# Performance work log

Measured on AMD Instinct MI355X. Metric: run time of the kernel, lower is better.

## Reference

```python
import jax, jax.numpy as jnp
import numpy as np

DIM = 512
MOVE_EMBED_DIM = 64
NUM_BUCKETS = 64
EMBED = 768
B = 8192
STEPS = 10


def setup_inputs() -> dict:
    key = jax.random.key(0)
    ks = jax.random.split(key, 16)
    def g(i, shape, scale=0.02):
        return jax.random.normal(ks[i], shape, jnp.float32) * scale
    return {
        "boards": jax.random.normal(ks[0], (STEPS, B, EMBED), jnp.float32),
        "flags": jax.random.randint(ks[1], (STEPS - 2, B), 0, 2).astype(bool),
        "themes": jax.random.randint(ks[2], (B,), 0, 10),
        "moves": jax.random.randint(ks[3], (B,), 0, NUM_BUCKETS),
        "start": jax.random.uniform(ks[4], (DIM,), jnp.float32),
        "red_w": g(5, (DIM, EMBED)), "red_b": jnp.zeros((DIM,), jnp.float32),
        "ca_w": g(6, (DIM, DIM)), "ca_b": jnp.zeros((DIM,), jnp.float32),
        "cb_w": g(7, (DIM, DIM)), "cb_b": jnp.zeros((DIM,), jnp.float32),
        "move_emb": g(8, (NUM_BUCKETS, MOVE_EMBED_DIM), 1.0),
        "fc1_w": g(9, (DIM, DIM + MOVE_EMBED_DIM)), "fc1_b": jnp.zeros((DIM,), jnp.float32),
        "fc2_w": g(10, (DIM, DIM)), "fc2_b": jnp.zeros((DIM,), jnp.float32),
        "fc3_w": g(11, (1024, DIM)), "fc3_b": jnp.zeros((1024,), jnp.float32),
        "fc4_w": g(12, (1024, 1024)), "fc4_b": jnp.zeros((1024,), jnp.float32),
        "fc5_w": g(13, (512, 1024)), "fc5_b": jnp.zeros((512,), jnp.float32),
        "out_w": g(14, (1, 512)), "out_b": jnp.zeros((1,), jnp.float32),
    }


def reference(boards, flags, themes, moves, start, red_w, red_b, ca_w, ca_b,
              cb_w, cb_b, move_emb, fc1_w, fc1_b, fc2_w, fc2_b, fc3_w, fc3_b,
              fc4_w, fc4_b, fc5_w, fc5_b, out_w, out_b):
    bsz = boards.shape[1]
    # boards[0:2] are never masked; boards[2:10] are zeroed where flags are False
    full_flags = jnp.concatenate([jnp.ones((2, bsz), bool), flags], axis=0)  # [10,B]
    emb = jnp.where(full_flags[:, :, None], boards, 0.0)                     # [10,B,E]
    # shared dim reducer + relu applied to all 10 positions at once
    e = jax.nn.relu(jnp.einsum('sbe,de->sbd', emb, red_w) + red_b)           # [10,B,DIM]
    # precompute combiner_b contribution for every step (batched GEMM)
    eb = jnp.einsum('sbd,kd->sbk', e, cb_w) + cb_b                           # [10,B,DIM]
    # combiner_a(start)+combiner_b(e0) == combiner_a(h0)+... with h0 = start broadcast
    h0 = jnp.broadcast_to(start, (bsz, DIM))
    def step(h, eb_t):
        return jnp.tanh(h @ ca_w.T + ca_b + eb_t), None
    h, _ = jax.lax.scan(step, h0, eb)                                        # [B,DIM]
    # dropout layers are identity in eval mode
    m = move_emb[moves]                                                      # [B,MOVE_EMBED_DIM]
    x = jax.nn.relu(jnp.concatenate([h, m], axis=-1) @ fc1_w.T + fc1_b)
    x = jax.nn.relu(x @ fc2_w.T + fc2_b)
    x = jax.nn.relu(x @ fc3_w.T + fc3_b)
    x = jax.nn.relu(x @ fc4_w.T + fc4_b)
    x = jax.nn.relu(x @ fc5_w.T + fc5_b)
    return x @ out_w.T + out_b                                               # [B,1]
```

## Files before the change

kernel.cpp:

```cpp
#include <hip/hip_runtime.h>
#include <math.h>

#define BATCH  8192
#define EMBED  768
#define DIMD   512
#define MEDIM  64
#define NSTEP  10

typedef __bf16 bf16x8 __attribute__((ext_vector_type(8)));
typedef float  f32x4  __attribute__((ext_vector_type(4)));

__device__ __forceinline__ void load16_lds(const void* g, void* l)
{
    auto* gp = (__attribute__((address_space(1))) char*)(uintptr_t)g;
    auto* lp = (__attribute__((address_space(3))) char*)(unsigned int)(uintptr_t)l;
    __builtin_amdgcn_global_load_lds(gp, lp, 16, 0, 0);
}

#define WAITV(n) asm volatile("s_waitcnt vmcnt(" #n ")" ::: "memory")

#define BN 128
#define BK 32

template<int ACT, bool ADDEB, bool GATHER, int BMT>
__global__ __launch_bounds__(256)
void gemm_bf16(const __bf16* __restrict__ A, const __bf16* __restrict__ Bt,
               const float* __restrict__ bias, const __bf16* __restrict__ add,
               const __bf16* __restrict__ me, const int* __restrict__ moves,
               __bf16* __restrict__ C, int M, int N, int K)
{
    constexpr int NG = (BMT + BN) / 16;
    constexpr int AG = BMT / 16;
    constexpr int MR = BMT / 32;
    constexpr int NC = NG / 4;

    __shared__ __bf16 lds[3][(BMT + BN) * BK];

    const int nwg  = gridDim.x * gridDim.y;
    const int orig = blockIdx.y * gridDim.x + blockIdx.x;
    const int cpx  = nwg >> 3;
    const int swz  = (orig & 7) * cpx + (orig >> 3);
    const int bx   = swz % gridDim.x;
    const int by   = swz / gridDim.x;

    const int tid  = threadIdx.x;
    const int wave = tid >> 6;
    const int lane = tid & 63;
    const int row0 = by * BMT;
    const int col0 = bx * BN;

    const int wr = (wave >> 1) * (BMT / 2);
    const int wc = (wave & 1) * 64;
    const int fr = lane & 15;
    const int q  = lane >> 4;

    const int srow = lane >> 2;
    const int skk  = (((lane & 3) ^ ((lane >> 3) & 3)) * 8);

    int mv[2] = {0, 0};
    if (GATHER) {
#pragma unroll
        for (int ci = 0; ci < 2; ++ci)
            mv[ci] = moves[row0 + (ci * 4 + wave) * 16 + srow];
    }

    auto stage_one = [&](int buf, int k0, int ci) {
        const int c = ci * 4 + wave;
        const int r = c * 16 + srow;
        const __bf16* g;
        if (c < AG) {
            if (GATHER) {
                g = (k0 < DIMD)
                    ? (A  + (size_t)(row0 + r) * DIMD + k0 + skk)
                    : (me + (size_t)mv[ci] * MEDIM + (k0 - DIMD) + skk);
            } else {
                g = A + (size_t)(row0 + r) * K + k0 + skk;
            }
        } else {
            g = Bt + (size_t)(col0 + (r - BMT)) * K + k0 + skk;
        }
        load16_lds(g, &lds[buf][c * 512]);
    };
    auto stage = [&](int buf, int k0) {
#pragma unroll
        for (int ci = 0; ci < NC; ++ci) stage_one(buf, k0, ci);
    };

    auto frag = [&](const __bf16* base, int r) -> bf16x8 {
        return *(const bf16x8*)&base[r * 32 + ((q ^ ((r >> 1) & 3)) << 3)];
    };

    f32x4 acc[MR][4] = {};

    const int NT = K / BK;
    stage(0, 0);
    stage(1, BK);

    int rd = 0;
    for (int t = 0; t < NT; ++t) {
        if (t + 1 < NT) {
            if constexpr (NC == 4) WAITV(4); else WAITV(3);
        } else {
            WAITV(0);
        }
        __builtin_amdgcn_s_barrier();
        __builtin_amdgcn_sched_barrier(0);

        const bool dost = (t + 2 < NT);
        int wrb = rd + 2; if (wrb >= 3) wrb -= 3;
        const int k0s = (t + 2) * BK;

        const __bf16* As = lds[rd];
        const __bf16* Bs = lds[rd] + BMT * BK;
        bf16x8 bfr[4];
#pragma unroll
        for (int n = 0; n < 4; ++n)
            bfr[n] = frag(Bs, wc + n * 16 + fr);

        __builtin_amdgcn_s_setprio(1);
#pragma unroll
        for (int m = 0; m < MR; ++m) {
            if (dost) {
#pragma unroll
                for (int ci = m * NC / MR; ci < (m + 1) * NC / MR; ++ci)
                    stage_one(wrb, k0s, ci);
            }
            const bf16x8 af = frag(As, wr + m * 16 + fr);
#pragma unroll
            for (int n = 0; n < 4; ++n)
                acc[m][n] = __builtin_amdgcn_mfma_f32_16x16x32_bf16(
                                af, bfr[n], acc[m][n], 0, 0, 0);
        }
        __builtin_amdgcn_s_setprio(0);

        __builtin_amdgcn_s_barrier();
        __builtin_amdgcn_sched_barrier(0);
        ++rd; if (rd >= 3) rd -= 3;
    }

#pragma unroll
    for (int m = 0; m < MR; ++m) {
#pragma unroll
        for (int n = 0; n < 4; ++n) {
            const int cc = col0 + wc + n * 16 + fr;
            const float bb = bias[cc];
#pragma unroll
            for (int j = 0; j < 4; ++j) {
                const int rr = row0 + wr + m * 16 + (lane >> 4) * 4 + j;
                float v = acc[m][n][j] + bb;
                if (ADDEB) v += (float)add[(size_t)rr * N + cc];
                if (ACT == 1) v = fmaxf(v, 0.0f);
                if (ACT == 2) {
                    const float p = __expf(2.0f * v);
                    v = 1.0f - 2.0f / (p + 1.0f);
                }
                C[(size_t)rr * N + cc] = (__bf16)v;
            }
        }
    }
}

template<int ACT, bool H1>
__global__ __launch_bounds__(512)
void gemm256(const __bf16* __restrict__ A, const __bf16* __restrict__ Bt,
             const float* __restrict__ bias, const float* __restrict__ tmp,
             __bf16* __restrict__ h1out, __bf16* __restrict__ C,
             int M, int N, int K)
{
    __shared__ __bf16 lds[3][(256 + 128) * 32];

    const int nwg  = gridDim.x * gridDim.y;
    const int orig = blockIdx.y * gridDim.x + blockIdx.x;
    const int cpx  = nwg >> 3;
    const int swz  = (orig & 7) * cpx + (orig >> 3);
    const int bx   = swz % gridDim.x;
    const int by   = swz / gridDim.x;

    const int tid  = threadIdx.x;
    const int wave = tid >> 6;
    const int lane = tid & 63;
    const int row0 = by * 256;
    const int col0 = bx * 128;

    const int wr = (wave >> 1) * 64;
    const int wc = (wave & 1) * 64;
    const int fr = lane & 15;
    const int q  = lane >> 4;

    const int srow = lane >> 2;
    const int skk  = (((lane & 3) ^ ((lane >> 3) & 3)) * 8);

    auto stage_one = [&](int buf, int k0, int ci) {
        const int c = ci * 8 + wave;
        const int r = c * 16 + srow;
        const __bf16* g = (c < 16)
            ? (A  + (size_t)(row0 + r) * K + k0 + skk)
            : (Bt + (size_t)(col0 + (r - 256)) * K + k0 + skk);
        load16_lds(g, &lds[buf][c * 512]);
    };
    auto stage = [&](int buf, int k0) {
#pragma unroll
        for (int ci = 0; ci < 3; ++ci) stage_one(buf, k0, ci);
    };

    auto frag = [&](const __bf16* base, int r) -> bf16x8 {
        return *(const bf16x8*)&base[r * 32 + ((q ^ ((r >> 1) & 3)) << 3)];
    };

    f32x4 acc[4][4] = {};

    const int NT = K / BK;
    stage(0, 0);
    stage(1, BK);

    int rd = 0;
    for (int t = 0; t < NT; ++t) {
        if (t + 1 < NT) WAITV(3); else WAITV(0);
        __builtin_amdgcn_s_barrier();
        __builtin_amdgcn_sched_barrier(0);

        const bool dost = (t + 2 < NT);
        int wrb = rd + 2; if (wrb >= 3) wrb -= 3;
        const int k0s = (t + 2) * BK;

        const __bf16* As = lds[rd];
        const __bf16* Bs = lds[rd] + 256 * 32;
        bf16x8 bfr[4];
#pragma unroll
        for (int n = 0; n < 4; ++n)
            bfr[n] = frag(Bs, wc + n * 16 + fr);

        __builtin_amdgcn_s_setprio(1);
#pragma unroll
        for (int m = 0; m < 4; ++m) {
            if (dost) {
#pragma unroll
                for (int ci = m * 3 / 4; ci < (m + 1) * 3 / 4; ++ci)
                    stage_one(wrb, k0s, ci);
            }
            const bf16x8 af = frag(As, wr + m * 16 + fr);
#pragma unroll
            for (int n = 0; n < 4; ++n)
                acc[m][n] = __builtin_amdgcn_mfma_f32_16x16x32_bf16(
                                af, bfr[n], acc[m][n], 0, 0, 0);
        }
        __builtin_amdgcn_s_setprio(0);

        __builtin_amdgcn_s_barrier();
        __builtin_amdgcn_sched_barrier(0);
        ++rd; if (rd >= 3) rd -= 3;
    }

#pragma unroll
    for (int m = 0; m < 4; ++m) {
#pragma unroll
        for (int n = 0; n < 4; ++n) {
            const int cc = col0 + wc + n * 16 + fr;
            const float bb = bias[cc];
#pragma unroll
            for (int j = 0; j < 4; ++j) {
                const int rr = row0 + wr + m * 16 + (lane >> 4) * 4 + j;
                float v = acc[m][n][j] + bb;
                if (ACT == 1) v = fmaxf(v, 0.0f);
                if (H1 && rr < BATCH) {
                    const float vv = v + tmp[cc];
                    const float p = __expf(2.0f * vv);
                    h1out[(size_t)rr * N + cc] = (__bf16)(1.0f - 2.0f / (p + 1.0f));
                } else {
                    C[(size_t)rr * N + cc] = (__bf16)v;
                }
            }
        }
    }
}

enum : int { W_RED = 0, W_CA = 393216, W_CB = 655360, W_FC1 = 917504,
             W_FC2 = 1212416, W_FC3 = 1474560, W_FC4 = 1998848,
             W_FC5 = 3047424, W_ME = 3571712, W_TOTAL = 3575808 };

#define NB_BOARDS 30720
#define NB_W      1746
__global__ __launch_bounds__(256)
void prep(const float* __restrict__ boards, const int* __restrict__ flags,
          __bf16* __restrict__ b_all,
          const float* __restrict__ w0, const float* __restrict__ w1,
          const float* __restrict__ w2, const float* __restrict__ w3,
          const float* __restrict__ w4, const float* __restrict__ w5,
          const float* __restrict__ w6, const float* __restrict__ w7,
          const float* __restrict__ w8, __bf16* __restrict__ wpool,
          const float* __restrict__ cab, const float* __restrict__ start,
          float* __restrict__ tmp)
{
    const int bid = blockIdx.x;
    if (bid < NB_BOARDS) {
        const int idx  = bid * 256 + threadIdx.x;
        const int grow = idx / 96;
        const int s    = grow >> 13;
        const int b    = grow & 8191;
        float m = 1.0f;
        if (s >= 2) m = flags[(size_t)(s - 2) * BATCH + b] ? 1.0f : 0.0f;
        const float4 v0 = ((const float4*)boards)[(size_t)idx * 2];
        const float4 v1 = ((const float4*)boards)[(size_t)idx * 2 + 1];
        bf16x8 o;
        o[0] = (__bf16)(v0.x * m); o[1] = (__bf16)(v0.y * m);
        o[2] = (__bf16)(v0.z * m); o[3] = (__bf16)(v0.w * m);
        o[4] = (__bf16)(v1.x * m); o[5] = (__bf16)(v1.y * m);
        o[6] = (__bf16)(v1.z * m); o[7] = (__bf16)(v1.w * m);
        *(bf16x8*)(b_all + (size_t)idx * 8) = o;
    } else if (bid < NB_BOARDS + NB_W) {
        const int idx = (bid - NB_BOARDS) * 256 + threadIdx.x;
        if (idx >= W_TOTAL / 8) return;
        const int e = idx * 8;
        const float* src; int off;
        if      (e < W_CA)  { src = w0; off = W_RED; }
        else if (e < W_CB)  { src = w1; off = W_CA; }
        else if (e < W_FC1) { src = w2; off = W_CB; }
        else if (e < W_FC2) { src = w3; off = W_FC1; }
        else if (e < W_FC3) { src = w4; off = W_FC2; }
        else if (e < W_FC4) { src = w5; off = W_FC3; }
        else if (e < W_FC5) { src = w6; off = W_FC4; }
        else if (e < W_ME)  { src = w7; off = W_FC5; }
        else                { src = w8; off = W_ME; }
        const float4 v0 = ((const float4*)(src + (e - off)))[0];
        const float4 v1 = ((const float4*)(src + (e - off)))[1];
        bf16x8 o;
        o[0] = (__bf16)v0.x; o[1] = (__bf16)v0.y; o[2] = (__bf16)v0.z; o[3] = (__bf16)v0.w;
        o[4] = (__bf16)v1.x; o[5] = (__bf16)v1.y; o[6] = (__bf16)v1.z; o[7] = (__bf16)v1.w;
        *(bf16x8*)(wpool + (size_t)e) = o;
    } else {
        __shared__ float s[DIMD];
        for (int i = threadIdx.x; i < DIMD; i += 256) s[i] = start[i];
        __syncthreads();
        const int n = (bid - NB_BOARDS - NB_W) * 256 + threadIdx.x;
        const float4* w = (const float4*)(w1 + (size_t)n * DIMD);
        float acc = 0.0f;
#pragma unroll 8
        for (int k = 0; k < DIMD / 4; ++k) {
            const float4 wv = w[k];
            acc += wv.x * s[k * 4] + wv.y * s[k * 4 + 1] +
                   wv.z * s[k * 4 + 2] + wv.w * s[k * 4 + 3];
        }
        tmp[n] = acc + cab[n];
    }
}

__global__ __launch_bounds__(256)
void out_head(const __bf16* __restrict__ x, const float* __restrict__ out_w,
              const float* __restrict__ out_b, float* __restrict__ out)
{
    const int wid  = threadIdx.x >> 6;
    const int lane = threadIdx.x & 63;
    const int row  = blockIdx.x * 4 + wid;
    const bf16x8 xv = *(const bf16x8*)(x + (size_t)row * DIMD + lane * 8);
    const float4 w0 = ((const float4*)out_w)[lane * 2];
    const float4 w1 = ((const float4*)out_w)[lane * 2 + 1];
    float s = (float)xv[0] * w0.x + (float)xv[1] * w0.y + (float)xv[2] * w0.z +
              (float)xv[3] * w0.w + (float)xv[4] * w1.x + (float)xv[5] * w1.y +
              (float)xv[6] * w1.z + (float)xv[7] * w1.w;
#pragma unroll
    for (int off = 32; off; off >>= 1) s += __shfl_down(s, off, 64);
    if (lane == 0) out[row] = s + out_b[0];
}

extern "C" void kernel_launch(void* const* d_in, const int* in_sizes, int n_in,
                              void* d_out, int out_size, void* d_ws, size_t ws_size,
                              hipStream_t stream)
{
    const float* boards  = (const float*)d_in[0];
    const int*   flags   = (const int*)  d_in[1];
    const int*   moves   = (const int*)  d_in[3];
    const float* start   = (const float*)d_in[4];
    const float* red_w   = (const float*)d_in[5];
    const float* red_b   = (const float*)d_in[6];
    const float* ca_w    = (const float*)d_in[7];
    const float* ca_b    = (const float*)d_in[8];
    const float* cb_w    = (const float*)d_in[9];
    const float* cb_b    = (const float*)d_in[10];
    const float* move_emb= (const float*)d_in[11];
    const float* fc1_w   = (const float*)d_in[12];
    const float* fc1_b   = (const float*)d_in[13];
    const float* fc2_w   = (const float*)d_in[14];
    const float* fc2_b   = (const float*)d_in[15];
    const float* fc3_w   = (const float*)d_in[16];
    const float* fc3_b   = (const float*)d_in[17];
    const float* fc4_w   = (const float*)d_in[18];
    const float* fc4_b   = (const float*)d_in[19];
    const float* fc5_w   = (const float*)d_in[20];
    const float* fc5_b   = (const float*)d_in[21];
    const float* out_w   = (const float*)d_in[22];
    const float* out_b   = (const float*)d_in[23];

    __bf16* wsb = (__bf16*)d_ws;
    __bf16* wpool  = wsb;
    __bf16* b_all  = wsb + 3575808;
    __bf16* e_all  = wsb + 66490368;
    __bf16* eb_all = wsb + 108433408;
    __bf16* hA     = wsb + 150376448;
    __bf16* hB     = wsb + 154570752;
    float*  tmpv   = (float*)(wsb + 158765056);
    __bf16* x1     = wsb + 159789056;
    __bf16* x2     = wsb + 163983360;
    __bf16* x3     = wsb + 168177664;
    __bf16* x4     = wsb + 176566272;
    __bf16* x5     = wsb + 184954880;

    const dim3 blk(256);

    prep<<<NB_BOARDS + NB_W + 2, blk, 0, stream>>>(
        boards, flags, b_all,
        red_w, ca_w, cb_w, fc1_w, fc2_w, fc3_w, fc4_w, fc5_w, move_emb, wpool,
        ca_b, start, tmpv);

    gemm256<1, false><<<dim3(4, 320), dim3(512), 0, stream>>>(
        b_all, wpool + W_RED, red_b, nullptr, nullptr, e_all,
        NSTEP * BATCH, DIMD, EMBED);
    gemm256<0, true><<<dim3(4, 320), dim3(512), 0, stream>>>(
        e_all, wpool + W_CB, cb_b, tmpv, hA, eb_all,
        NSTEP * BATCH, DIMD, DIMD);

    __bf16* hcur = hA;
    __bf16* hnxt = hB;
    for (int s = 1; s < NSTEP; ++s) {
        const __bf16* ebs = eb_all + (size_t)s * BATCH * DIMD;
        gemm_bf16<2, true, false, 64><<<dim3(4, 128), blk, 0, stream>>>(
            hcur, wpool + W_CA, ca_b, ebs, nullptr, nullptr, hnxt,
            BATCH, DIMD, DIMD);
        __bf16* t = hcur; hcur = hnxt; hnxt = t;
    }

    gemm_bf16<1, false, true, 128><<<dim3(4, 64), blk, 0, stream>>>(
        hcur, wpool + W_FC1, fc1_b, nullptr, wpool + W_ME, moves, x1,
        BATCH, DIMD, DIMD + MEDIM);
    gemm_bf16<1, false, false, 128><<<dim3(4, 64), blk, 0, stream>>>(
        x1, wpool + W_FC2, fc2_b, nullptr, nullptr, nullptr, x2, BATCH, DIMD, DIMD);
    gemm_bf16<1, false, false, 128><<<dim3(8, 64), blk, 0, stream>>>(
        x2, wpool + W_FC3, fc3_b, nullptr, nullptr, nullptr, x3, BATCH, 1024, DIMD);
    gemm_bf16<1, false, false, 128><<<dim3(8, 64), blk, 0, stream>>>(
        x3, wpool + W_FC4, fc4_b, nullptr, nullptr, nullptr, x4, BATCH, 1024, 1024);
    gemm_bf16<1, false, false, 128><<<dim3(4, 64), blk, 0, stream>>>(
        x4, wpool + W_FC5, fc5_b, nullptr, nullptr, nullptr, x5, BATCH, DIMD, 1024);

    out_head<<<BATCH / 4, blk, 0, stream>>>(x5, out_w, out_b, (float*)d_out);
}
```

Measured before the change: 437.7 us.

## Use 256x256-tile ping-pong GEMM kernel for the board reducer

Adds a new gemm8p kernel with 256x256 output tiles, a triple-buffered LDS pipeline in dynamic shared memory, and global-to-LDS loads interleaved with MFMA phases separated by barriers and setprio. The reducer GEMM (81920x768 -> 512) now uses it, halving the column blocks, so each A row tile is loaded once per 256 columns instead of once per 128. This reduces global traffic and raises arithmetic intensity. In exchange it needs a large per-block accumulator set (128 floats per lane) and about 96 KB of LDS, which limits occupancy to one block per CU.

Result: no change. 437.4 us (median of 3 runs) (-0.1%).

```diff
diff --git a/kernel.cpp b/kernel.cpp
--- a/kernel.cpp
+++ b/kernel.cpp
@@ -154,6 +154,113 @@
                     const float p = __expf(2.0f * v);
                     v = 1.0f - 2.0f / (p + 1.0f);
                 }
+                C[(size_t)rr * N + cc] = (__bf16)v;
+            }
+        }
+    }
+}
+
+template<int ACT>
+__global__ __launch_bounds__(512)
+void gemm8p(const __bf16* __restrict__ A, const __bf16* __restrict__ Bt,
+            const float* __restrict__ bias, __bf16* __restrict__ C,
+            int M, int N, int K)
+{
+    extern __shared__ __bf16 dyn[];
+
+    const int nwg  = gridDim.x * gridDim.y;
+    const int orig = blockIdx.y * gridDim.x + blockIdx.x;
+    const int cpx  = nwg >> 3;
+    const int swz  = (orig & 7) * cpx + (orig >> 3);
+    const int bx   = swz % gridDim.x;
+    const int by   = swz / gridDim.x;
+
+    const int tid  = threadIdx.x;
+    const int wave = tid >> 6;
+    const int lane = tid & 63;
+    const int row0 = by * 256;
+    const int col0 = bx * 256;
+
+    const int wr = (wave >> 2) * 128;
+    const int wc = (wave & 3) * 64;
+    const int fr = lane & 15;
+    const int q  = lane >> 4;
+
+    const int srow = lane >> 2;
+    const int skk  = (((lane & 3) ^ ((lane >> 3) & 3)) * 8);
+
+    auto stage_one = [&](int buf, int k0, int ci) {
+        const int c = ci * 8 + wave;
+        const int r = c * 16 + srow;
+        const __bf16* g = (c < 16)
+            ? (A  + (size_t)(row0 + r) * K + k0 + skk)
+            : (Bt + (size_t)(col0 + (r - 256)) * K + k0 + skk);
+        load16_lds(g, &dyn[buf * 16384 + c * 512]);
+    };
+    auto stage = [&](int buf, int k0) {
+#pragma unroll
+        for (int ci = 0; ci < 4; ++ci) stage_one(buf, k0, ci);
+    };
+
+    auto frag = [&](const __bf16* base, int r) -> bf16x8 {
+        return *(const bf16x8*)&base[r * 32 + ((q ^ ((r >> 1) & 3)) << 3)];
+    };
+
+    f32x4 acc[8][4] = {};
+
+    const int NT = K / BK;
+    stage(0, 0);
+    stage(1, BK);
+
+    int rd = 0;
+    for (int t = 0; t < NT; ++t) {
+        if (t + 1 < NT) WAITV(4); else WAITV(0);
+        __builtin_amdgcn_s_barrier();
+        __builtin_amdgcn_sched_barrier(0);
+
+        const bool dost = (t + 2 < NT);
+        int wrb = rd + 2; if (wrb >= 3) wrb -= 3;
+        const int k0s = (t + 2) * BK;
+
+        const __bf16* As = dyn + rd * 16384;
+        const __bf16* Bs = As + 256 * 32;
+        bf16x8 bfr[4];
+#pragma unroll
+        for (int n = 0; n < 4; ++n)
+            bfr[n] = frag(Bs, wc + n * 16 + fr);
+
+#pragma unroll
+        for (int p = 0; p < 4; ++p) {
+            if (dost) stage_one(wrb, k0s, p);
+            const bf16x8 af0 = frag(As, wr + (2 * p)     * 16 + fr);
+            const bf16x8 af1 = frag(As, wr + (2 * p + 1) * 16 + fr);
+            __builtin_amdgcn_s_setprio(1);
+#pragma unroll
+            for (int n = 0; n < 4; ++n)
+                acc[2 * p][n] = __builtin_amdgcn_mfma_f32_16x16x32_bf16(
+                                    af0, bfr[n], acc[2 * p][n], 0, 0, 0);
+#pragma unroll
+            for (int n = 0; n < 4; ++n)
+                acc[2 * p + 1][n] = __builtin_amdgcn_mfma_f32_16x16x32_bf16(
+                                        af1, bfr[n], acc[2 * p + 1][n], 0, 0, 0);
+            __builtin_amdgcn_s_setprio(0);
+            __builtin_amdgcn_s_barrier();
+            __builtin_amdgcn_sched_barrier(0);
+        }
+        ++rd; if (rd >= 3) rd -= 3;
+    }
+
+#pragma unroll
+    for (int m = 0; m < 8; ++m) {
+#pragma unroll
+        for (int n = 0; n < 4; ++n) {
+            const int cc = col0 + wc + n * 16 + fr;
+            const float bb = bias[cc];
+#pragma unroll
+            for (int j = 0; j < 4; ++j) {
+                const int rr = row0 + wr + m * 16 + (lane >> 4) * 4 + j;
+                float v = acc[m][n][j] + bb;
+                if (ACT == 1) v = fmaxf(v, 0.0f);
                 C[(size_t)rr * N + cc] = (__bf16)v;
             }
         }
@@ -405,15 +512,15 @@
     __bf16* x5     = wsb + 184954880;
 
     const dim3 blk(256);
+    const size_t LDS8P = 3 * 16384 * sizeof(__bf16);
 
     prep<<<NB_BOARDS + NB_W + 2, blk, 0, stream>>>(
         boards, flags, b_all,
         red_w, ca_w, cb_w, fc1_w, fc2_w, fc3_w, fc4_w, fc5_w, move_emb, wpool,
         ca_b, start, tmpv);
 
-    gemm256<1, false><<<dim3(4, 320), dim3(512), 0, stream>>>(
-        b_all, wpool + W_RED, red_b, nullptr, nullptr, e_all,
-        NSTEP * BATCH, DIMD, EMBED);
+    gemm8p<1><<<dim3(2, 320), dim3(512), LDS8P, stream>>>(
+        b_all, wpool + W_RED, red_b, e_all, NSTEP * BATCH, DIMD, EMBED);
     gemm256<0, true><<<dim3(4, 320), dim3(512), 0, stream>>>(
         e_all, wpool + W_CB, cb_b, tmpv, hA, eb_all,
         NSTEP * BATCH, DIMD, DIMD);
```
